# Kernel tuning notes

Hardware: AMD Instinct MI355X
Metric: run time of the kernel (lower is better)

The kernel has to match this reference:

```python
import jax, jax.numpy as jnp
import numpy as np

B, N, E, L, S = 8, 64, 256, 128, 2  # graphs, nodes, edges, latent dim, MPN steps


def setup_inputs() -> dict:
    key = jax.random.key(0)
    ks = jax.random.split(key, 16)

    def lin(k, fi, fo):
        return (jax.random.normal(k, (fi, fo), jnp.float32) / np.sqrt(fi).astype(np.float32))

    return {
        "x": jax.random.normal(ks[0], (B, N, L), jnp.float32),
        "edge_attr": jax.random.normal(ks[1], (B, E, L), jnp.float32),
        "u": jax.random.normal(ks[2], (B, L), jnp.float32),
        "spdist": jax.random.uniform(ks[3], (B, N, N), jnp.float32),
        "edge_index": jax.random.randint(ks[4], (B, 2, E), 0, N),
        # encoders
        "W_node_enc": lin(ks[5], 2 * L + 1, L), "b_node_enc": jnp.zeros(L, jnp.float32),
        "W_edge_enc": lin(ks[6], L, L), "b_edge_enc": jnp.zeros(L, jnp.float32),
        "W_glob_enc": lin(ks[7], L, L), "b_glob_enc": jnp.zeros(L, jnp.float32),
        # per-step edge / node update MLPs (stacked over S steps)
        "W_edge_upd": jnp.stack([lin(ks[8 + s], 4 * L, L) for s in range(S)]),
        "b_edge_upd": jnp.zeros((S, L), jnp.float32),
        "W_node_upd": jnp.stack([lin(ks[10 + s], 3 * L, L) for s in range(S)]),
        "b_node_upd": jnp.zeros((S, L), jnp.float32),
        # final edge scorer (per_dest_embedding_to_score)
        "W_score": lin(ks[12], L, 1), "b_score": jnp.zeros(1, jnp.float32),
    }


def reference(x, edge_attr, u, spdist, edge_index,
              W_node_enc, b_node_enc, W_edge_enc, b_edge_enc,
              W_glob_enc, b_glob_enc, W_edge_upd, b_edge_upd,
              W_node_upd, b_node_upd, W_score, b_score):
    act = jax.nn.leaky_relu  # torch LeakyReLU default slope 0.01
    n_steps = W_edge_upd.shape[0]

    def per_graph(xg, eg, ug, sdg, eig):
        Ng, Lg = xg.shape
        Eg = eg.shape[0]
        src, dst = eig[0], eig[1]
        # Augmented node features: graph copy d, node i -> [x_i, x_d, spdist[d, i]]
        # (matches x.repeat(N,1) / x.repeat_interleave(N,0) + chunk(N))
        x_tile = jnp.broadcast_to(xg[None, :, :], (Ng, Ng, Lg))
        x_dest = jnp.broadcast_to(xg[:, None, :], (Ng, Ng, Lg))
        xa = jnp.concatenate([x_tile, x_dest, sdg[..., None]], axis=-1)  # [Nd, N, 2L+1]
        h = act(xa @ W_node_enc + b_node_enc)                            # [Nd, N, L]
        ee = act(eg @ W_edge_enc + b_edge_enc)                           # [E, L]
        ee = jnp.broadcast_to(ee[None], (Ng, Eg, Lg))                    # [Nd, E, L]
        gg = act(ug @ W_glob_enc + b_glob_enc)                           # [L]
        for s in range(n_steps):
            gb_e = jnp.broadcast_to(gg, (Ng, Eg, Lg))
            ein = jnp.concatenate([ee, h[:, src], h[:, dst], gb_e], axis=-1)  # [Nd, E, 4L]
            ee = ee + act(ein @ W_edge_upd[s] + b_edge_upd[s])
            agg = jax.vmap(lambda ef: jax.ops.segment_sum(ef, dst, num_segments=Ng))(ee)  # [Nd, N, L]
            gb_n = jnp.broadcast_to(gg, (Ng, Ng, Lg))
            nin = jnp.concatenate([h, agg, gb_n], axis=-1)                    # [Nd, N, 3L]
            h = h + act(nin @ W_node_upd[s] + b_node_upd[s])
        scores = (ee @ W_score + b_score)[..., 0]  # [Nd, E]
        # reshape(N, -1).t().flatten() per graph -> [E * N]
        return scores.T.reshape(-1)

    out = jax.vmap(per_graph)(x, edge_attr, u, spdist, edge_index)  # [B, E*N]
    return out.reshape(-1)
```

## Files before the change

### kernel.cpp

```cpp
#include <hip/hip_runtime.h>
#include <hip/hip_bf16.h>


typedef __attribute__((ext_vector_type(8))) __bf16 bf16x8;
typedef __attribute__((ext_vector_type(4))) __bf16 bf16x4;
typedef __attribute__((ext_vector_type(4))) float  floatx4;

#define MFMA16(a, b, c) __builtin_amdgcn_mfma_f32_16x16x32_bf16((a), (b), (c), 0, 0, 0)

__device__ __forceinline__ float leaky(float x) { return x > 0.f ? x : 0.01f * x; }

#define WS_WT     0
#define WS_XAP    327680
#define WS_XDP    589824
#define WS_EE0    851968
#define WS_CE     1376256
#define WS_CN     1384448
#define WS_CSROFF 1392640
#define WS_CSREID 1394944

#define LDE 140

__global__ __launch_bounds__(256) void mpn_prep(
    const float* __restrict__ x,
    const float* __restrict__ ea,
    const float* __restrict__ u,
    const int*   __restrict__ eidx,
    const float* __restrict__ Wne,
    const float* __restrict__ bne,
    const float* __restrict__ Wee,
    const float* __restrict__ bee,
    const float* __restrict__ Wge,
    const float* __restrict__ bge,
    const float* __restrict__ Weu,
    const float* __restrict__ beu,
    const float* __restrict__ Wnu,
    const float* __restrict__ bnu,
    char* __restrict__ ws)
{
  __shared__ __align__(16) __bf16 smem[384 * LDE];

  const int b = blockIdx.x, tid = threadIdx.x;
  __bf16* wt  = (__bf16*)(ws + WS_WT);
  float*  xap = (float*)(ws + WS_XAP);
  float*  xdp = (float*)(ws + WS_XDP);
  __bf16* ee0 = (__bf16*)(ws + WS_EE0);
  float*  cev = (float*)(ws + WS_CE);
  float*  cnv = (float*)(ws + WS_CN);
  int* csroff = (int*)(ws + WS_CSROFF);
  int* csreid = (int*)(ws + WS_CSREID);

  if (b < 20) {
    const int m = b >> 1, half = b & 1;
    const int s = m / 5, t = m % 5;
    const float* src = (t < 3) ? (Weu + (size_t)(s*512 + t*128)*128)
                               : (Wnu + (size_t)(s*384 + (t-3)*128)*128);
    for (int it = 0; it < 4; ++it) {
      int p = it*256 + tid;
      int mq = half*4 + (p >> 8);
      int c  = (p >> 6) & 3;
      int l  = p & 63;
      int fr = mq*16 + (l & 15);
      int kb = c*32 + (l >> 4)*8;
      __bf16* dst = &wt[m*16384 + ((mq*4 + c)*64 + l)*8];
      #pragma unroll
      for (int j = 0; j < 8; ++j)
        dst[j] = (__bf16)src[(kb + j)*128 + fr];
    }
  } else if (b < 28) {
    const int g = b - 20;
    __shared__ float gg_sh[128];
    __shared__ int dst_sh[256];
    __shared__ int cnt_sh[64];
    __shared__ int off_sh[65];
    if (tid < 128) {
      float acc = bge[tid];
      for (int k = 0; k < 128; ++k)
        acc += u[g*128 + k] * Wge[k*128 + tid];
      gg_sh[tid] = leaky(acc);
    }
    dst_sh[tid] = eidx[g*512 + 256 + tid];
    __syncthreads();
    {
      const int s = tid >> 7, f = tid & 127;
      float ac = beu[s*128 + f];
      float an = bnu[s*128 + f];
      #pragma unroll 8
      for (int k = 0; k < 128; ++k) {
        float gk = gg_sh[k];
        ac += gk * Weu[(s*512 + 384 + k)*128 + f];
        an += gk * Wnu[(s*384 + 256 + k)*128 + f];
      }
      cev[(g*2 + s)*128 + f] = ac;
      cnv[(g*2 + s)*128 + f] = an;
    }
    if (tid < 64) {
      int c = 0;
      for (int e = 0; e < 256; ++e) c += (dst_sh[e] == tid) ? 1 : 0;
      cnt_sh[tid] = c;
    }
    __syncthreads();
    if (tid == 0) {
      int o = 0;
      for (int n = 0; n < 64; ++n) { off_sh[n] = o; o += cnt_sh[n]; }
      off_sh[64] = o;
    }
    __syncthreads();
    if (tid < 65) csroff[g*72 + tid] = off_sh[tid];
    if (tid < 64) {
      int o = off_sh[tid];
      for (int e = 0; e < 256; ++e)
        if (dst_sh[e] == tid) csreid[g*256 + (o++)] = e;
    }
  } else if (b < 36) {
    const int g = b - 28;
    __bf16* s_a = smem;
    __bf16* s_w = smem + 256*LDE;
    #pragma unroll
    for (int it = 0; it < 32; ++it) {
      int c = it*256 + tid;
      int row = c >> 5, f4 = (c & 31)*4;
      floatx4 v = *(const floatx4*)&ea[(size_t)(g*256 + row)*128 + f4];
      bf16x4 o;
      #pragma unroll
      for (int r = 0; r < 4; ++r) o[r] = (__bf16)v[r];
      *(bf16x4*)&s_a[row*LDE + f4] = o;
    }
    #pragma unroll 8
    for (int it = 0; it < 64; ++it) {
      int k = it*2 + (tid >> 7), f = tid & 127;
      s_w[f*LDE + k] = (__bf16)Wee[k*128 + f];
    }
    __syncthreads();
    const int w = tid >> 6, l = tid & 63, q = l >> 4, xn = l & 15;
    bf16x8 bea[4][4];
    #pragma unroll
    for (int t = 0; t < 4; ++t) {
      int e = w*64 + t*16 + xn;
      #pragma unroll
      for (int c = 0; c < 4; ++c)
        bea[t][c] = *(const bf16x8*)&s_a[e*LDE + c*32 + q*8];
    }
    #pragma unroll
    for (int m = 0; m < 8; ++m) {
      floatx4 acc[4];
      #pragma unroll
      for (int t = 0; t < 4; ++t) acc[t] = (floatx4)0.f;
      const int fr = m*16 + xn;
      #pragma unroll
      for (int c = 0; c < 4; ++c) {
        bf16x8 aw = *(const bf16x8*)&s_w[fr*LDE + c*32 + q*8];
        #pragma unroll
        for (int t = 0; t < 4; ++t) acc[t] = MFMA16(aw, bea[t][c], acc[t]);
      }
      const int f0 = m*16 + q*4;
      floatx4 b4 = *(const floatx4*)&bee[f0];
      #pragma unroll
      for (int t = 0; t < 4; ++t) {
        int e = w*64 + t*16 + xn;
        bf16x4 o;
        #pragma unroll
        for (int r = 0; r < 4; ++r) o[r] = (__bf16)leaky(acc[t][r] + b4[r]);
        *(bf16x4*)&ee0[(size_t)(g*256 + e)*128 + f0] = o;
      }
    }
  } else {
    const int g = b - 36;
    __bf16* s_x  = smem;
    __bf16* s_wa = smem + 64*LDE;
    __bf16* s_wb = smem + 192*LDE;
    #pragma unroll
    for (int it = 0; it < 8; ++it) {
      int c = it*256 + tid;
      int row = c >> 5, f4 = (c & 31)*4;
      floatx4 v = *(const floatx4*)&x[(size_t)(g*64 + row)*128 + f4];
      bf16x4 o;
      #pragma unroll
      for (int r = 0; r < 4; ++r) o[r] = (__bf16)v[r];
      *(bf16x4*)&s_x[row*LDE + f4] = o;
    }
    #pragma unroll 8
    for (int it = 0; it < 64; ++it) {
      int k = it*2 + (tid >> 7), f = tid & 127;
      s_wa[f*LDE + k] = (__bf16)Wne[k*128 + f];
      s_wb[f*LDE + k] = (__bf16)Wne[(128 + k)*128 + f];
    }
    __syncthreads();
    const int w = tid >> 6, l = tid & 63, q = l >> 4, xn = l & 15;
    const int i = w*16 + xn;
    bf16x8 bx[4];
    #pragma unroll
    for (int c = 0; c < 4; ++c)
      bx[c] = *(const bf16x8*)&s_x[i*LDE + c*32 + q*8];
    #pragma unroll
    for (int m = 0; m < 8; ++m) {
      floatx4 aa = (floatx4)0.f, ab = (floatx4)0.f;
      const int fr = m*16 + xn;
      #pragma unroll
      for (int c = 0; c < 4; ++c) {
        bf16x8 aw = *(const bf16x8*)&s_wa[fr*LDE + c*32 + q*8];
        aa = MFMA16(aw, bx[c], aa);
      }
      #pragma unroll
      for (int c = 0; c < 4; ++c) {
        bf16x8 aw = *(const bf16x8*)&s_wb[fr*LDE + c*32 + q*8];
        ab = MFMA16(aw, bx[c], ab);
      }
      const int f0 = m*16 + q*4;
      floatx4 bn4 = *(const floatx4*)&bne[f0];
      floatx4 oa;
      #pragma unroll
      for (int r = 0; r < 4; ++r) oa[r] = aa[r] + bn4[r];
      *(floatx4*)&xap[(size_t)(g*64 + i)*128 + f0] = oa;
      *(floatx4*)&xdp[(size_t)(g*64 + i)*128 + f0] = ab;
    }
  }
}

__global__ __launch_bounds__(512, 2) void mpn_main(
    const float* __restrict__ spdist,
    const int*   __restrict__ eidx,
    const float* __restrict__ Wne,
    const float* __restrict__ wscore,
    const float* __restrict__ bscore,
    const char* __restrict__ ws,
    float* __restrict__ out)
{
  __shared__ __align__(16) __bf16 s_ee[256*LDE];
  __shared__ __align__(16) __bf16 s_h [64*LDE];
  __shared__ __align__(16) __bf16 s_p2[64*LDE];
  __shared__ __align__(16) __bf16 s_p3[64*LDE];
  __shared__ int s_off[65];
  __shared__ int s_eid[256];
  __shared__ float s_sc[256];

  const __bf16* wt  = (const __bf16*)(ws + WS_WT);
  const float*  xap = (const float*)(ws + WS_XAP);
  const float*  xdp = (const float*)(ws + WS_XDP);
  const __bf16* ee0 = (const __bf16*)(ws + WS_EE0);
  const float*  cev = (const float*)(ws + WS_CE);
  const float*  cnv = (const float*)(ws + WS_CN);
  const int* csroff = (const int*)(ws + WS_CSROFF);
  const int* csreid = (const int*)(ws + WS_CSREID);

  const int tid = threadIdx.x;
  const int w = tid >> 6, l = tid & 63;
  const int q = l >> 4, xn = l & 15;
  const int wp = w >> 1, mh = w & 1;
  const int lane8 = l*8;
  const int fme = w*16 + q*4;
  const int g = blockIdx.x >> 6, d = blockIdx.x & 63;

  if (tid < 65) s_off[tid] = csroff[g*72 + tid];
  if (tid < 256) s_eid[tid] = csreid[g*256 + tid];

  {
    const int f = tid & 127, ib = tid >> 7;
    float xdpv = xdp[(g*64 + d)*128 + f];
    float wspv = Wne[256*128 + f];
    #pragma unroll
    for (int j = 0; j < 16; ++j) {
      int i = ib + 4*j;
      float sp = spdist[(g*64 + d)*64 + i];
      float v = xap[(g*64 + i)*128 + f] + xdpv + sp*wspv;
      s_h[i*LDE + f] = (__bf16)leaky(v);
    }
  }
  #pragma unroll
  for (int it = 0; it < 8; ++it) {
    int c = it*512 + tid;
    int row = c >> 4, col = c & 15;
    *(bf16x8*)&s_ee[row*LDE + col*8] = *(const bf16x8*)&ee0[(g*256 + row)*128 + col*8];
  }

  int mySrc[4], myDst[4];
  #pragma unroll
  for (int t = 0; t < 4; ++t) {
    int e = wp*64 + t*16 + xn;
    mySrc[t] = eidx[g*512 + e];
    myDst[t] = eidx[g*512 + 256 + e];
  }
  __syncthreads();

  for (int s = 0; s < 2; ++s) {
    const __bf16* W1T = wt + (s*5 + 0)*16384;
    const __bf16* W2T = wt + (s*5 + 1)*16384;
    const __bf16* W3T = wt + (s*5 + 2)*16384;
    const __bf16* N1T = wt + (s*5 + 3)*16384;
    const __bf16* N2T = wt + (s*5 + 4)*16384;

    bf16x8 w2f[4], w3f[4], n1f[4], n2f[4], w1f[4][4];
    #pragma unroll
    for (int c = 0; c < 4; ++c) {
      w2f[c] = *(const bf16x8*)&W2T[(w*4 + c)*512 + lane8];
      w3f[c] = *(const bf16x8*)&W3T[(w*4 + c)*512 + lane8];
    }
    #pragma unroll
    for (int mm = 0; mm < 4; ++mm)
      #pragma unroll
      for (int c = 0; c < 4; ++c)
        w1f[mm][c] = *(const bf16x8*)&W1T[((mh*4 + mm)*4 + c)*512 + lane8];
    if (s == 0) {
      #pragma unroll
      for (int c = 0; c < 4; ++c) {
        n1f[c] = *(const bf16x8*)&N1T[(w*4 + c)*512 + lane8];
        n2f[c] = *(const bf16x8*)&N2T[(w*4 + c)*512 + lane8];
      }
    }

    {
      floatx4 ce4 = *(const floatx4*)&cev[(g*2 + s)*128 + fme];
      #pragma unroll
      for (int t = 0; t < 4; ++t) {
        const int i = t*16 + xn;
        floatx4 a2 = (floatx4)0.f, a3 = (floatx4)0.f;
        #pragma unroll
        for (int c = 0; c < 4; ++c) {
          bf16x8 bh = *(const bf16x8*)&s_h[i*LDE + c*32 + q*8];
          a2 = MFMA16(w2f[c], bh, a2);
          a3 = MFMA16(w3f[c], bh, a3);
        }
        bf16x4 o2, o3;
        #pragma unroll
        for (int r = 0; r < 4; ++r) { o2[r] = (__bf16)a2[r]; o3[r] = (__bf16)(a3[r] + ce4[r]); }
        *(bf16x4*)&s_p2[i*LDE + fme] = o2;
        *(bf16x4*)&s_p3[i*LDE + fme] = o3;
      }
    }
    __syncthreads();

    {
      bf16x8 be[4][4];
      #pragma unroll
      for (int t = 0; t < 4; ++t) {
        int e = wp*64 + t*16 + xn;
        #pragma unroll
        for (int c = 0; c < 4; ++c)
          be[t][c] = *(const bf16x8*)&s_ee[e*LDE + c*32 + q*8];
      }
      __syncthreads();
      #pragma unroll
      for (int mm = 0; mm < 4; ++mm) {
        const int m = mh*4 + mm;
        floatx4 acc[4];
        #pragma unroll
        for (int t = 0; t < 4; ++t) acc[t] = (floatx4)0.f;
        #pragma unroll
        for (int c = 0; c < 4; ++c) {
          #pragma unroll
          for (int t = 0; t < 4; ++t) acc[t] = MFMA16(w1f[mm][c], be[t][c], acc[t]);
        }
        const int f0 = m*16 + q*4;
        #pragma unroll
        for (int t = 0; t < 4; ++t) {
          int e = wp*64 + t*16 + xn;
          bf16x4 old = *(const bf16x4*)&s_ee[e*LDE + f0];
          bf16x4 v2  = *(const bf16x4*)&s_p2[mySrc[t]*LDE + f0];
          bf16x4 v3  = *(const bf16x4*)&s_p3[myDst[t]*LDE + f0];
          bf16x4 res;
          #pragma unroll
          for (int r = 0; r < 4; ++r) {
            float vv = acc[t][r] + (float)v2[r] + (float)v3[r];
            res[r] = (__bf16)((float)old[r] + leaky(vv));
          }
          *(bf16x4*)&s_ee[e*LDE + f0] = res;
        }
      }
    }
    __syncthreads();

    if (s == 0) {
      {
        const int node = tid >> 3;
        const int fs = (tid & 7)*16;
        float av[16];
        #pragma unroll
        for (int j = 0; j < 16; ++j) av[j] = 0.f;
        const int b0 = s_off[node], b1 = s_off[node + 1];
        for (int idx = b0; idx < b1; ++idx) {
          int e = s_eid[idx];
          #pragma unroll
          for (int cc = 0; cc < 2; ++cc) {
            bf16x8 vv = *(const bf16x8*)&s_ee[e*LDE + fs + cc*8];
            #pragma unroll
            for (int j = 0; j < 8; ++j) av[cc*8 + j] += (float)vv[j];
          }
        }
        #pragma unroll
        for (int cc = 0; cc < 2; ++cc) {
          bf16x8 o;
          #pragma unroll
          for (int j = 0; j < 8; ++j) o[j] = (__bf16)av[cc*8 + j];
          *(bf16x8*)&s_p2[node*LDE + fs + cc*8] = o;
        }
      }
      __syncthreads();
      {
        floatx4 acc4[4];
        #pragma unroll
        for (int t = 0; t < 4; ++t) {
          const int i = t*16 + xn;
          floatx4 a = (floatx4)0.f;
          #pragma unroll
          for (int c = 0; c < 4; ++c) {
            bf16x8 bh = *(const bf16x8*)&s_h[i*LDE + c*32 + q*8];
            a = MFMA16(n1f[c], bh, a);
          }
          #pragma unroll
          for (int c = 0; c < 4; ++c) {
            bf16x8 bg = *(const bf16x8*)&s_p2[i*LDE + c*32 + q*8];
            a = MFMA16(n2f[c], bg, a);
          }
          acc4[t] = a;
        }
        __syncthreads();
        floatx4 cn4 = *(const floatx4*)&cnv[(g*2 + s)*128 + fme];
        #pragma unroll
        for (int t = 0; t < 4; ++t) {
          const int i = t*16 + xn;
          bf16x4 old = *(const bf16x4*)&s_h[i*LDE + fme];
          bf16x4 res;
          #pragma unroll
          for (int r = 0; r < 4; ++r)
            res[r] = (__bf16)((float)old[r] + leaky(acc4[t][r] + cn4[r]));
          *(bf16x4*)&s_h[i*LDE + fme] = res;
        }
      }
      __syncthreads();
    }
  }

  {
    const int e = tid & 255, hh = tid >> 8;
    float acc = 0.f;
    #pragma unroll
    for (int c = 0; c < 8; ++c) {
      bf16x8 vv = *(const bf16x8*)&s_ee[e*LDE + hh*64 + c*8];
      #pragma unroll
      for (int j = 0; j < 8; ++j) acc += (float)vv[j] * wscore[hh*64 + c*8 + j];
    }
    if (hh == 1) s_sc[e] = acc;
    __syncthreads();
    if (hh == 0) out[g*16384 + e*64 + d] = acc + s_sc[e] + bscore[0];
  }
}

extern "C" void kernel_launch(void* const* d_in, const int* in_sizes, int n_in,
                              void* d_out, int out_size, void* d_ws, size_t ws_size,
                              hipStream_t stream) {
  (void)in_sizes; (void)n_in; (void)out_size; (void)ws_size;
  const float* x   = (const float*)d_in[0];
  const float* ea  = (const float*)d_in[1];
  const float* u   = (const float*)d_in[2];
  const float* sp  = (const float*)d_in[3];
  const int*   ei  = (const int*)d_in[4];
  const float* Wne = (const float*)d_in[5];
  const float* bne = (const float*)d_in[6];
  const float* Wee = (const float*)d_in[7];
  const float* bee = (const float*)d_in[8];
  const float* Wge = (const float*)d_in[9];
  const float* bge = (const float*)d_in[10];
  const float* Weu = (const float*)d_in[11];
  const float* beu = (const float*)d_in[12];
  const float* Wnu = (const float*)d_in[13];
  const float* bnu = (const float*)d_in[14];
  const float* Wsc = (const float*)d_in[15];
  const float* bsc = (const float*)d_in[16];
  char* ws = (char*)d_ws;

  hipLaunchKernelGGL(mpn_prep, dim3(44), dim3(256), 0, stream,
                     x, ea, u, ei, Wne, bne, Wee, bee, Wge, bge, Weu, beu, Wnu, bnu, ws);
  hipLaunchKernelGGL(mpn_main, dim3(512), dim3(512), 0, stream,
                     sp, ei, Wne, Wsc, bsc, (const char*)ws, (float*)d_out);
}
```

Measured before the change: 155.1 us.

## Precompute step-0 edge-feature GEMM once per graph in prep kernel

Step 0's ee@W1 product is identical for all 64 destination copies of a graph, because ee starts from the shared encoder output. The prep kernel now computes it once per graph and writes it to the workspace in fp32. The main kernel's step 0 then skips the W1 MFMA and only adds the precomputed product to the gathered node projections. This removes 64x redundant matmul work in step 0, at the cost of extra prep work and reading a fp32 buffer per block from global memory.

```diff
diff --git a/kernel.cpp b/kernel.cpp
--- a/kernel.cpp
+++ b/kernel.cpp
@@ -18,6 +18,7 @@
 #define WS_CN     1384448
 #define WS_CSROFF 1392640
 #define WS_CSREID 1394944
+#define WS_EW0    1403136
 
 #define LDE 140
 
@@ -116,6 +117,7 @@
     const int g = b - 28;
     __bf16* s_a = smem;
     __bf16* s_w = smem + 256*LDE;
+    float* ew0 = (float*)(ws + WS_EW0);
     #pragma unroll
     for (int it = 0; it < 32; ++it) {
       int c = it*256 + tid;
@@ -162,6 +164,41 @@
         #pragma unroll
         for (int r = 0; r < 4; ++r) o[r] = (__bf16)leaky(acc[t][r] + b4[r]);
         *(bf16x4*)&ee0[(size_t)(g*256 + e)*128 + f0] = o;
+        *(bf16x4*)&s_a[e*LDE + f0] = o;
+      }
+    }
+    __syncthreads();
+    #pragma unroll 8
+    for (int it = 0; it < 64; ++it) {
+      int k = it*2 + (tid >> 7), f = tid & 127;
+      s_w[f*LDE + k] = (__bf16)Weu[k*128 + f];
+    }
+    __syncthreads();
+    bf16x8 beb[4][4];
+    #pragma unroll
+    for (int t = 0; t < 4; ++t) {
+      int e = w*64 + t*16 + xn;
+      #pragma unroll
+      for (int c = 0; c < 4; ++c)
+        beb[t][c] = *(const bf16x8*)&s_a[e*LDE + c*32 + q*8];
+    }
+    #pragma unroll
+    for (int m = 0; m < 8; ++m) {
+      floatx4 acc[4];
+      #pragma unroll
+      for (int t = 0; t < 4; ++t) acc[t] = (floatx4)0.f;
+      const int fr = m*16 + xn;
+      #pragma unroll
+      for (int c = 0; c < 4; ++c) {
+        bf16x8 aw = *(const bf16x8*)&s_w[fr*LDE + c*32 + q*8];
+        #pragma unroll
+        for (int t = 0; t < 4; ++t) acc[t] = MFMA16(aw, beb[t][c], acc[t]);
+      }
+      const int f0 = m*16 + q*4;
+      #pragma unroll
+      for (int t = 0; t < 4; ++t) {
+        int e = w*64 + t*16 + xn;
+        *(floatx4*)&ew0[((size_t)g*256 + e)*128 + f0] = acc[t];
       }
     }
   } else {
@@ -240,6 +277,7 @@
   const __bf16* ee0 = (const __bf16*)(ws + WS_EE0);
   const float*  cev = (const float*)(ws + WS_CE);
   const float*  cnv = (const float*)(ws + WS_CN);
+  const float*  ew0 = (const float*)(ws + WS_EW0);
   const int* csroff = (const int*)(ws + WS_CSROFF);
   const int* csreid = (const int*)(ws + WS_CSREID);
 
@@ -265,12 +303,6 @@
       float v = xap[(g*64 + i)*128 + f] + xdpv + sp*wspv;
       s_h[i*LDE + f] = (__bf16)leaky(v);
     }
-  }
-  #pragma unroll
-  for (int it = 0; it < 8; ++it) {
-    int c = it*512 + tid;
-    int row = c >> 4, col = c & 15;
-    *(bf16x8*)&s_ee[row*LDE + col*8] = *(const bf16x8*)&ee0[(g*256 + row)*128 + col*8];
   }
 
   int mySrc[4], myDst[4];
@@ -295,11 +327,13 @@
       w2f[c] = *(const bf16x8*)&W2T[(w*4 + c)*512 + lane8];
       w3f[c] = *(const bf16x8*)&W3T[(w*4 + c)*512 + lane8];
     }
-    #pragma unroll
-    for (int mm = 0; mm < 4; ++mm)
-      #pragma unroll
-      for (int c = 0; c < 4; ++c)
-        w1f[mm][c] = *(const bf16x8*)&W1T[((mh*4 + mm)*4 + c)*512 + lane8];
+    if (s == 1) {
+      #pragma unroll
+      for (int mm = 0; mm < 4; ++mm)
+        #pragma unroll
+        for (int c = 0; c < 4; ++c)
+          w1f[mm][c] = *(const bf16x8*)&W1T[((mh*4 + mm)*4 + c)*512 + lane8];
+    }
     if (s == 0) {
       #pragma unroll
       for (int c = 0; c < 4; ++c) {
@@ -329,7 +363,28 @@
     }
     __syncthreads();
 
-    {
+    if (s == 0) {
+      #pragma unroll
+      for (int mm = 0; mm < 4; ++mm) {
+        const int m = mh*4 + mm;
+        const int f0 = m*16 + q*4;
+        #pragma unroll
+        for (int t = 0; t < 4; ++t) {
+          int e = wp*64 + t*16 + xn;
+          floatx4 ew  = *(const floatx4*)&ew0[((size_t)g*256 + e)*128 + f0];
+          bf16x4 old  = *(const bf16x4*)&ee0[(size_t)(g*256 + e)*128 + f0];
+          bf16x4 v2   = *(const bf16x4*)&s_p2[mySrc[t]*LDE + f0];
+          bf16x4 v3   = *(const bf16x4*)&s_p3[myDst[t]*LDE + f0];
+          bf16x4 res;
+          #pragma unroll
+          for (int r = 0; r < 4; ++r) {
+            float vv = ew[r] + (float)v2[r] + (float)v3[r];
+            res[r] = (__bf16)((float)old[r] + leaky(vv));
+          }
+          *(bf16x4*)&s_ee[e*LDE + f0] = res;
+        }
+      }
+    } else {
       bf16x8 be[4][4];
       #pragma unroll
       for (int t = 0; t < 4; ++t) {
```

New measurement: 173.0 us. 11.6% more time.

## Fuse final edge scoring into last edge-update epilogue and reorder block-to-graph mapping

Applied to the files above, without the earlier changes.

In the last message-passing step, the edge update no longer writes the new edge embeddings back to shared memory. Instead it dots them with the score weights in registers, reduces across lanes with shuffles, and stores per-wave partial scores. This drops one barrier, the final LDS write-back, and the separate scoring pass. The block index mapping is also changed so that consecutive blocks cover different graphs rather than different destination nodes of one graph, which alters cache locality and the output write pattern.

```diff
diff --git a/kernel.cpp b/kernel.cpp
--- a/kernel.cpp
+++ b/kernel.cpp
@@ -232,7 +232,7 @@
   __shared__ __align__(16) __bf16 s_p3[64*LDE];
   __shared__ int s_off[65];
   __shared__ int s_eid[256];
-  __shared__ float s_sc[256];
+  __shared__ float s_scp[512];
 
   const __bf16* wt  = (const __bf16*)(ws + WS_WT);
   const float*  xap = (const float*)(ws + WS_XAP);
@@ -249,7 +249,7 @@
   const int wp = w >> 1, mh = w & 1;
   const int lane8 = l*8;
   const int fme = w*16 + q*4;
-  const int g = blockIdx.x >> 6, d = blockIdx.x & 63;
+  const int g = blockIdx.x & 7, d = blockIdx.x >> 3;
 
   if (tid < 65) s_off[tid] = csroff[g*72 + tid];
   if (tid < 256) s_eid[tid] = csreid[g*256 + tid];
@@ -290,6 +290,7 @@
     const __bf16* N2T = wt + (s*5 + 4)*16384;
 
     bf16x8 w2f[4], w3f[4], n1f[4], n2f[4], w1f[4][4];
+    floatx4 wsf[4];
     #pragma unroll
     for (int c = 0; c < 4; ++c) {
       w2f[c] = *(const bf16x8*)&W2T[(w*4 + c)*512 + lane8];
@@ -306,6 +307,10 @@
         n1f[c] = *(const bf16x8*)&N1T[(w*4 + c)*512 + lane8];
         n2f[c] = *(const bf16x8*)&N2T[(w*4 + c)*512 + lane8];
       }
+    } else {
+      #pragma unroll
+      for (int mm = 0; mm < 4; ++mm)
+        wsf[mm] = *(const floatx4*)&wscore[(mh*4 + mm)*16 + q*4];
     }
 
     {
@@ -338,32 +343,68 @@
         for (int c = 0; c < 4; ++c)
           be[t][c] = *(const bf16x8*)&s_ee[e*LDE + c*32 + q*8];
       }
-      __syncthreads();
-      #pragma unroll
-      for (int mm = 0; mm < 4; ++mm) {
-        const int m = mh*4 + mm;
-        floatx4 acc[4];
-        #pragma unroll
-        for (int t = 0; t < 4; ++t) acc[t] = (floatx4)0.f;
-        #pragma unroll
-        for (int c = 0; c < 4; ++c) {
-          #pragma unroll
-          for (int t = 0; t < 4; ++t) acc[t] = MFMA16(w1f[mm][c], be[t][c], acc[t]);
-        }
-        const int f0 = m*16 + q*4;
+      if (s == 0) {
+        __syncthreads();
+        #pragma unroll
+        for (int mm = 0; mm < 4; ++mm) {
+          const int m = mh*4 + mm;
+          floatx4 acc[4];
+          #pragma unroll
+          for (int t = 0; t < 4; ++t) acc[t] = (floatx4)0.f;
+          #pragma unroll
+          for (int c = 0; c < 4; ++c) {
+            #pragma unroll
+            for (int t = 0; t < 4; ++t) acc[t] = MFMA16(w1f[mm][c], be[t][c], acc[t]);
+          }
+          const int f0 = m*16 + q*4;
+          #pragma unroll
+          for (int t = 0; t < 4; ++t) {
+            int e = wp*64 + t*16 + xn;
+            bf16x4 old = *(const bf16x4*)&s_ee[e*LDE + f0];
+            bf16x4 v2  = *(const bf16x4*)&s_p2[mySrc[t]*LDE + f0];
+            bf16x4 v3  = *(const bf16x4*)&s_p3[myDst[t]*LDE + f0];
+            bf16x4 res;
+            #pragma unroll
+            for (int r = 0; r < 4; ++r) {
+              float vv = acc[t][r] + (float)v2[r] + (float)v3[r];
+              res[r] = (__bf16)((float)old[r] + leaky(vv));
+            }
+            *(bf16x4*)&s_ee[e*LDE + f0] = res;
+          }
+        }
+      } else {
+        float sc[4] = {0.f, 0.f, 0.f, 0.f};
+        #pragma unroll
+        for (int mm = 0; mm < 4; ++mm) {
+          const int m = mh*4 + mm;
+          floatx4 acc[4];
+          #pragma unroll
+          for (int t = 0; t < 4; ++t) acc[t] = (floatx4)0.f;
+          #pragma unroll
+          for (int c = 0; c < 4; ++c) {
+            #pragma unroll
+            for (int t = 0; t < 4; ++t) acc[t] = MFMA16(w1f[mm][c], be[t][c], acc[t]);
+          }
+          const int f0 = m*16 + q*4;
+          #pragma unroll
+          for (int t = 0; t < 4; ++t) {
+            int e = wp*64 + t*16 + xn;
+            bf16x4 old = *(const bf16x4*)&s_ee[e*LDE + f0];
+            bf16x4 v2  = *(const bf16x4*)&s_p2[mySrc[t]*LDE + f0];
+            bf16x4 v3  = *(const bf16x4*)&s_p3[myDst[t]*LDE + f0];
+            #pragma unroll
+            for (int r = 0; r < 4; ++r) {
+              float vv = acc[t][r] + (float)v2[r] + (float)v3[r];
+              sc[t] += ((float)old[r] + leaky(vv)) * wsf[mm][r];
+            }
+          }
+        }
         #pragma unroll
         for (int t = 0; t < 4; ++t) {
-          int e = wp*64 + t*16 + xn;
-          bf16x4 old = *(const bf16x4*)&s_ee[e*LDE + f0];
-          bf16x4 v2  = *(const bf16x4*)&s_p2[mySrc[t]*LDE + f0];
-          bf16x4 v3  = *(const bf16x4*)&s_p3[myDst[t]*LDE + f0];
-          bf16x4 res;
-          #pragma unroll
-          for (int r = 0; r < 4; ++r) {
-            float vv = acc[t][r] + (float)v2[r] + (float)v3[r];
-            res[r] = (__bf16)((float)old[r] + leaky(vv));
-          }
-          *(bf16x4*)&s_ee[e*LDE + f0] = res;
+          float v = sc[t];
+          v += __shfl_xor(v, 16);
+          v += __shfl_xor(v, 32);
+          if (l < 16) s_scp[w*64 + t*16 + l] = v;
         }
       }
     }
@@ -430,18 +471,10 @@
     }
   }
 
-  {
-    const int e = tid & 255, hh = tid >> 8;
-    float acc = 0.f;
-    #pragma unroll
-    for (int c = 0; c < 8; ++c) {
-      bf16x8 vv = *(const bf16x8*)&s_ee[e*LDE + hh*64 + c*8];
-      #pragma unroll
-      for (int j = 0; j < 8; ++j) acc += (float)vv[j] * wscore[hh*64 + c*8 + j];
-    }
-    if (hh == 1) s_sc[e] = acc;
-    __syncthreads();
-    if (hh == 0) out[g*16384 + e*64 + d] = acc + s_sc[e] + bscore[0];
+  if (tid < 256) {
+    const int e = tid, wpair = e >> 6, wi = e & 63;
+    out[g*16384 + e*64 + d] =
+        s_scp[(wpair*2)*64 + wi] + s_scp[(wpair*2 + 1)*64 + wi] + bscore[0];
   }
 }
 
```

Result: slower. 202.2 us (+30.4%).

## Double mpn_main block to 1024 threads and split per-wave work in half

Applied to the files above, without the earlier changes.

Launches the main kernel with 1024 threads (16 waves) per block instead of 512 and re-partitions the work so each wave handles half as many node/edge tiles. Node-projection tiles are now split by feature tile and node half, and the edge tiles are split into 32-edge chunks. The final scoring switches to a 4-lane shuffle reduction, which removes one shared buffer and a barrier. The aim is more waves in flight to hide LDS and MFMA latency. In exchange, launch bounds drop from 2 blocks to 1 block per CU, each wave gets more registers, and weight fragments are now loaded redundantly by twice as many waves.

```diff
diff --git a/kernel.cpp b/kernel.cpp
--- a/kernel.cpp
+++ b/kernel.cpp
@@ -217,7 +217,7 @@
   }
 }
 
-__global__ __launch_bounds__(512, 2) void mpn_main(
+__global__ __launch_bounds__(1024, 1) void mpn_main(
     const float* __restrict__ spdist,
     const int*   __restrict__ eidx,
     const float* __restrict__ Wne,
@@ -232,7 +232,6 @@
   __shared__ __align__(16) __bf16 s_p3[64*LDE];
   __shared__ int s_off[65];
   __shared__ int s_eid[256];
-  __shared__ float s_sc[256];
 
   const __bf16* wt  = (const __bf16*)(ws + WS_WT);
   const float*  xap = (const float*)(ws + WS_XAP);
@@ -246,9 +245,12 @@
   const int tid = threadIdx.x;
   const int w = tid >> 6, l = tid & 63;
   const int q = l >> 4, xn = l & 15;
-  const int wp = w >> 1, mh = w & 1;
+  const int wp = w >> 1;
+  const int mh = w & 1;
+  const int m8 = w >> 1;
+  const int nh = w & 1;
   const int lane8 = l*8;
-  const int fme = w*16 + q*4;
+  const int fme = m8*16 + q*4;
   const int g = blockIdx.x >> 6, d = blockIdx.x & 63;
 
   if (tid < 65) s_off[tid] = csroff[g*72 + tid];
@@ -259,24 +261,24 @@
     float xdpv = xdp[(g*64 + d)*128 + f];
     float wspv = Wne[256*128 + f];
     #pragma unroll
-    for (int j = 0; j < 16; ++j) {
-      int i = ib + 4*j;
+    for (int j = 0; j < 8; ++j) {
+      int i = ib + 8*j;
       float sp = spdist[(g*64 + d)*64 + i];
       float v = xap[(g*64 + i)*128 + f] + xdpv + sp*wspv;
       s_h[i*LDE + f] = (__bf16)leaky(v);
     }
   }
   #pragma unroll
-  for (int it = 0; it < 8; ++it) {
-    int c = it*512 + tid;
+  for (int it = 0; it < 4; ++it) {
+    int c = it*1024 + tid;
     int row = c >> 4, col = c & 15;
     *(bf16x8*)&s_ee[row*LDE + col*8] = *(const bf16x8*)&ee0[(g*256 + row)*128 + col*8];
   }
 
-  int mySrc[4], myDst[4];
+  int mySrc[2], myDst[2];
   #pragma unroll
-  for (int t = 0; t < 4; ++t) {
-    int e = wp*64 + t*16 + xn;
+  for (int t = 0; t < 2; ++t) {
+    int e = wp*32 + t*16 + xn;
     mySrc[t] = eidx[g*512 + e];
     myDst[t] = eidx[g*512 + 256 + e];
   }
@@ -292,8 +294,8 @@
     bf16x8 w2f[4], w3f[4], n1f[4], n2f[4], w1f[4][4];
     #pragma unroll
     for (int c = 0; c < 4; ++c) {
-      w2f[c] = *(const bf16x8*)&W2T[(w*4 + c)*512 + lane8];
-      w3f[c] = *(const bf16x8*)&W3T[(w*4 + c)*512 + lane8];
+      w2f[c] = *(const bf16x8*)&W2T[(m8*4 + c)*512 + lane8];
+      w3f[c] = *(const bf16x8*)&W3T[(m8*4 + c)*512 + lane8];
     }
     #pragma unroll
     for (int mm = 0; mm < 4; ++mm)
@@ -303,16 +305,16 @@
     if (s == 0) {
       #pragma unroll
       for (int c = 0; c < 4; ++c) {
-        n1f[c] = *(const bf16x8*)&N1T[(w*4 + c)*512 + lane8];
-        n2f[c] = *(const bf16x8*)&N2T[(w*4 + c)*512 + lane8];
+        n1f[c] = *(const bf16x8*)&N1T[(m8*4 + c)*512 + lane8];
+        n2f[c] = *(const bf16x8*)&N2T[(m8*4 + c)*512 + lane8];
       }
     }
 
     {
       floatx4 ce4 = *(const floatx4*)&cev[(g*2 + s)*128 + fme];
       #pragma unroll
-      for (int t = 0; t < 4; ++t) {
-        const int i = t*16 + xn;
+      for (int t = 0; t < 2; ++t) {
+        const int i = nh*32 + t*16 + xn;
         floatx4 a2 = (floatx4)0.f, a3 = (floatx4)0.f;
         #pragma unroll
         for (int c = 0; c < 4; ++c) {
@@ -330,10 +332,10 @@
     __syncthreads();
 
     {
-      bf16x8 be[4][4];
-      #pragma unroll
-      for (int t = 0; t < 4; ++t) {
-        int e = wp*64 + t*16 + xn;
+      bf16x8 be[2][4];
+      #pragma unroll
+      for (int t = 0; t < 2; ++t) {
+        int e = wp*32 + t*16 + xn;
         #pragma unroll
         for (int c = 0; c < 4; ++c)
           be[t][c] = *(const bf16x8*)&s_ee[e*LDE + c*32 + q*8];
@@ -342,18 +344,18 @@
       #pragma unroll
       for (int mm = 0; mm < 4; ++mm) {
         const int m = mh*4 + mm;
-        floatx4 acc[4];
-        #pragma unroll
-        for (int t = 0; t < 4; ++t) acc[t] = (floatx4)0.f;
+        floatx4 acc[2];
+        #pragma unroll
+        for (int t = 0; t < 2; ++t) acc[t] = (floatx4)0.f;
         #pragma unroll
         for (int c = 0; c < 4; ++c) {
           #pragma unroll
-          for (int t = 0; t < 4; ++t) acc[t] = MFMA16(w1f[mm][c], be[t][c], acc[t]);
+          for (int t = 0; t < 2; ++t) acc[t] = MFMA16(w1f[mm][c], be[t][c], acc[t]);
         }
         const int f0 = m*16 + q*4;
         #pragma unroll
-        for (int t = 0; t < 4; ++t) {
-          int e = wp*64 + t*16 + xn;
+        for (int t = 0; t < 2; ++t) {
+          int e = wp*32 + t*16 + xn;
           bf16x4 old = *(const bf16x4*)&s_ee[e*LDE + f0];
           bf16x4 v2  = *(const bf16x4*)&s_p2[mySrc[t]*LDE + f0];
           bf16x4 v3  = *(const bf16x4*)&s_p3[myDst[t]*LDE + f0];
@@ -371,35 +373,29 @@
 
     if (s == 0) {
       {
-        const int node = tid >> 3;
-        const int fs = (tid & 7)*16;
-        float av[16];
-        #pragma unroll
-        for (int j = 0; j < 16; ++j) av[j] = 0.f;
+        const int node = tid >> 4;
+        const int fs = (tid & 15)*8;
+        float av[8];
+        #pragma unroll
+        for (int j = 0; j < 8; ++j) av[j] = 0.f;
         const int b0 = s_off[node], b1 = s_off[node + 1];
         for (int idx = b0; idx < b1; ++idx) {
           int e = s_eid[idx];
-          #pragma unroll
-          for (int cc = 0; cc < 2; ++cc) {
-            bf16x8 vv = *(const bf16x8*)&s_ee[e*LDE + fs + cc*8];
-            #pragma unroll
-            for (int j = 0; j < 8; ++j) av[cc*8 + j] += (float)vv[j];
-          }
-        }
-        #pragma unroll
-        for (int cc = 0; cc < 2; ++cc) {
-          bf16x8 o;
-          #pragma unroll
-          for (int j = 0; j < 8; ++j) o[j] = (__bf16)av[cc*8 + j];
-          *(bf16x8*)&s_p2[node*LDE + fs + cc*8] = o;
-        }
+          bf16x8 vv = *(const bf16x8*)&s_ee[e*LDE + fs];
+          #pragma unroll
+          for (int j = 0; j < 8; ++j) av[j] += (float)vv[j];
+        }
+        bf16x8 o;
+        #pragma unroll
+        for (int j = 0; j < 8; ++j) o[j] = (__bf16)av[j];
+        *(bf16x8*)&s_p2[node*LDE + fs] = o;
       }
       __syncthreads();
       {
-        floatx4 acc4[4];
-        #pragma unroll
-        for (int t = 0; t < 4; ++t) {
-          const int i = t*16 + xn;
+        floatx4 acc4[2];
+        #pragma unroll
+        for (int t = 0; t < 2; ++t) {
+          const int i = nh*32 + t*16 + xn;
           floatx4 a = (floatx4)0.f;
           #pragma unroll
           for (int c = 0; c < 4; ++c) {
@@ -416,8 +412,8 @@
         __syncthreads();
         floatx4 cn4 = *(const floatx4*)&cnv[(g*2 + s)*128 + fme];
         #pragma unroll
-        for (int t = 0; t < 4; ++t) {
-          const int i = t*16 + xn;
+        for (int t = 0; t < 2; ++t) {
+          const int i = nh*32 + t*16 + xn;
           bf16x4 old = *(const bf16x4*)&s_h[i*LDE + fme];
           bf16x4 res;
           #pragma unroll
@@ -431,17 +427,17 @@
   }
 
   {
-    const int e = tid & 255, hh = tid >> 8;
+    const int e = tid >> 2, qq = tid & 3;
     float acc = 0.f;
     #pragma unroll
-    for (int c = 0; c < 8; ++c) {
-      bf16x8 vv = *(const bf16x8*)&s_ee[e*LDE + hh*64 + c*8];
-      #pragma unroll
-      for (int j = 0; j < 8; ++j) acc += (float)vv[j] * wscore[hh*64 + c*8 + j];
-    }
-    if (hh == 1) s_sc[e] = acc;
-    __syncthreads();
-    if (hh == 0) out[g*16384 + e*64 + d] = acc + s_sc[e] + bscore[0];
+    for (int c = 0; c < 4; ++c) {
+      bf16x8 vv = *(const bf16x8*)&s_ee[e*LDE + qq*32 + c*8];
+      #pragma unroll
+      for (int j = 0; j < 8; ++j) acc += (float)vv[j] * wscore[qq*32 + c*8 + j];
+    }
+    acc += __shfl_xor(acc, 1);
+    acc += __shfl_xor(acc, 2);
+    if (qq == 0) out[g*16384 + e*64 + d] = acc + bscore[0];
   }
 }
 
@@ -470,6 +466,6 @@
 
   hipLaunchKernelGGL(mpn_prep, dim3(44), dim3(256), 0, stream,
                      x, ea, u, ei, Wne, bne, Wee, bee, Wge, bge, Weu, beu, Wnu, bnu, ws);
-  hipLaunchKernelGGL(mpn_main, dim3(512), dim3(512), 0, stream,
+  hipLaunchKernelGGL(mpn_main, dim3(512), dim3(1024), 0, stream,
                      sp, ei, Wne, Wsc, bsc, (const char*)ws, (float*)d_out);
 }
```

Result: slower. 176.6 us (+13.9%).
